# Kernel optimization log

Measured on AMD Instinct MI355X. Metric: run time of the kernel, lower is better.

## Reference

```python
import jax, jax.numpy as jnp
import numpy as np

N_ENT = 100000
N_REL = 500
IN_DIM = 128
OUT_DIM = 128
E = 500000


def setup_inputs() -> dict:
    key = jax.random.key(0)
    ks = jax.random.split(key, 9)
    src = jax.random.randint(ks[0], (E,), 0, N_ENT)
    dst = jax.random.randint(ks[1], (E,), 0, N_ENT)
    rel = jax.random.randint(ks[2], (E,), 0, N_REL)
    ent_embed = jax.random.normal(ks[3], (N_ENT, IN_DIM), dtype=jnp.float32)
    rel_embed = jax.random.normal(ks[4], (N_REL, IN_DIM), dtype=jnp.float32)
    # xavier_normal with gain 1.414 for linear weights
    g = 1.414
    a_w = jax.random.normal(ks[5], (OUT_DIM, 3 * IN_DIM), dtype=jnp.float32) * (g * np.sqrt(2.0 / (3 * IN_DIM + OUT_DIM)))
    a_b = jnp.zeros((OUT_DIM,), dtype=jnp.float32)
    a2_w = jax.random.normal(ks[6], (1, OUT_DIM), dtype=jnp.float32) * (g * np.sqrt(2.0 / (OUT_DIM + 1)))
    a2_b = jnp.zeros((1,), dtype=jnp.float32)
    return {"ent_embed": ent_embed, "rel_embed": rel_embed, "a_w": a_w, "a_b": a_b,
            "a2_w": a2_w, "a2_b": a2_b, "src": src, "dst": dst, "rel": rel}


def reference(ent_embed, rel_embed, a_w, a_b, a2_w, a2_b, src, dst, rel):
    # gather: [E, 3*in_dim]
    h = jnp.concatenate([ent_embed[src], ent_embed[dst], rel_embed[rel]], axis=1)
    c = h @ a_w.T + a_b                      # [E, out_dim]
    b = jax.nn.leaky_relu(c @ a2_w.T + a2_b, negative_slope=0.01)  # [E, 1]
    e_b = jnp.exp(b)                          # [E, 1]
    temp1 = e_b * c                           # [E, out_dim]
    # scatter-sum into source nodes (SpecialSpmmFinal keyed on edges[0] = src)
    e_b_sum = jax.ops.segment_sum(e_b, src, num_segments=N_ENT)   # [N, 1]
    h_sum = jax.ops.segment_sum(temp1, src, num_segments=N_ENT)   # [N, out_dim]
    ebs = jnp.where(e_b_sum == 0, jnp.float32(1e-12), e_b_sum)
    h_ent = h_sum / ebs
    # scatter-mean of temp1 by relation id
    rel_sum = jax.ops.segment_sum(temp1, rel, num_segments=N_REL)          # [R, out_dim]
    rel_cnt = jax.ops.segment_sum(jnp.ones((temp1.shape[0],), jnp.float32), rel, num_segments=N_REL)
    h_rel = rel_sum / jnp.maximum(rel_cnt, 1.0)[:, None]
    return (jax.nn.elu(h_ent), jax.nn.elu(h_rel))
```

## Files before the change

### kernel.cpp

```cpp
#include <hip/hip_runtime.h>
#include <hip/hip_bf16.h>

#define N_ENT_C 100000
#define N_REL_C 500
#define NEDGE_C 500000
#define SCAN_BLOCKS 391
#define EPB 1024
#define NB_EDGE 489
#define CHUNK_B 62
#define MT_TOTAL 6250
#define MT_PER_BLOCK 8
#define MFMA_GRID 782
#define CVT_GRID 1563

#define OFF_WTHI  0
#define OFF_WTLO  16384
#define OFF_WTR   32768
#define OFF_PR    49152
#define OFF_PRH   113152
#define OFF_QR    145920
#define OFF_QS    146432
#define OFF_QD    246432
#define OFF_OSRC  346432
#define OFF_DRE   446432
#define OFF_PSH   2446432
#define OFF_PDH   8846432

#define DO_HSRC     0
#define DO_BSUM     100000
#define DO_RELSTART 100512
#define DO_PART8    101024
#define DO_CHUNKOFF 105120
#define DO_BLKHIST  109216
#define DO_BLKOFFS  359584
#define DO_SDE      609952
#define DO_RELP     2609952

typedef short bf16x8 __attribute__((ext_vector_type(8)));
typedef float f32x4  __attribute__((ext_vector_type(4)));
typedef float f32x2  __attribute__((ext_vector_type(2)));
typedef unsigned short u16x8 __attribute__((ext_vector_type(8)));

__device__ inline unsigned short bf_rne(float x) {
    unsigned int u = __float_as_uint(x);
    u += 0x7FFF + ((u >> 16) & 1);
    return (unsigned short)(u >> 16);
}
__device__ inline float bf2f(unsigned short h) {
    return __uint_as_float(((unsigned int)h) << 16);
}
__device__ inline f32x2 bfpair(unsigned int w) {
    f32x2 r;
    r.x = __uint_as_float(w << 16);
    r.y = __uint_as_float(w & 0xFFFF0000u);
    return r;
}

__global__ void prep_w(const float* __restrict__ aw, unsigned short* __restrict__ Wthi,
                       unsigned short* __restrict__ Wtlo, float* __restrict__ Wtr) {
    int idx = blockIdx.x * 256 + threadIdx.x;
    if (idx < 32768) {
        int n = idx >> 7, k = idx & 127;
        float v = (n < 128) ? aw[n * 384 + k] : aw[(n - 128) * 384 + 128 + k];
        unsigned short h = bf_rne(v);
        Wthi[idx] = h;
        Wtlo[idx] = bf_rne(v - bf2f(h));
    } else if (idx < 49152) {
        int t = idx - 32768;
        int k = t >> 7, o = t & 127;
        Wtr[t] = aw[o * 384 + 256 + k];
    }
}

__global__ void rel_proj(const float* __restrict__ rele, const float* __restrict__ Wtr,
                         const float* __restrict__ ab, const float* __restrict__ a2w,
                         float* __restrict__ Pr, unsigned short* __restrict__ PrH,
                         float* __restrict__ qr) {
    int r = blockIdx.x;
    int o = threadIdx.x;
    float acc = ab[o];
    for (int k = 0; k < 128; ++k)
        acc = fmaf(rele[r * 128 + k], Wtr[k * 128 + o], acc);
    Pr[r * 128 + o] = acc;
    PrH[r * 128 + o] = bf_rne(acc);
    __shared__ float red[128];
    red[o] = acc * a2w[o];
    __syncthreads();
    for (int off = 64; off > 0; off >>= 1) {
        if (o < off) red[o] += red[o + off];
        __syncthreads();
    }
    if (o == 0) qr[r] = red[0];
}

__global__ __launch_bounds__(256) void ent_cvt(const float* __restrict__ ent,
                                               uint4* __restrict__ EntF) {
    int gw = blockIdx.x * 256 + threadIdx.x;
    int mt = gw >> 6;
    if (mt >= MT_TOTAL) return;
    int lane = gw & 63;
    int row = mt * 16 + (lane & 15);
    int kb0 = (lane >> 4) * 8;
    const float* rp = ent + (size_t)row * 128;
    size_t mb = (size_t)mt * 8;
#pragma unroll
    for (int ks = 0; ks < 4; ++ks) {
        float4 a = *(const float4*)(rp + ks * 32 + kb0);
        float4 b = *(const float4*)(rp + ks * 32 + kb0 + 4);
        float f[8] = {a.x, a.y, a.z, a.w, b.x, b.y, b.z, b.w};
        union { unsigned short u[8]; uint4 v; } H, L;
#pragma unroll
        for (int j = 0; j < 8; ++j) {
            unsigned short h = bf_rne(f[j]);
            H.u[j] = h;
            L.u[j] = bf_rne(f[j] - bf2f(h));
        }
        EntF[(mb + ks) * 64 + lane] = H.v;
        EntF[(mb + 4 + ks) * 64 + lane] = L.v;
    }
}

__global__ __launch_bounds__(512, 4) void ent_mfma3(const uint4* __restrict__ EntF,
                                                    const unsigned short* __restrict__ Wthi,
                                                    const unsigned short* __restrict__ Wtlo,
                                                    const float* __restrict__ a2w,
                                                    unsigned short* __restrict__ PsH,
                                                    unsigned short* __restrict__ PdH,
                                                    float* __restrict__ qs,
                                                    float* __restrict__ qd) {
    const int tid = threadIdx.x;
    const int w = tid >> 6, lane = tid & 63;
    const int l15 = lane & 15, lh = lane >> 4;
    const int n0 = w * 32;

    bf16x8 wh[2][4], wl[2][4];
#pragma unroll
    for (int nf = 0; nf < 2; ++nf) {
        int n = n0 + nf * 16 + l15;
#pragma unroll
        for (int ks = 0; ks < 4; ++ks) {
            int kb = ks * 32 + lh * 8;
            wh[nf][ks] = *(const bf16x8*)(Wthi + n * 128 + kb);
            wl[nf][ks] = *(const bf16x8*)(Wtlo + n * 128 + kb);
        }
    }
#pragma unroll
    for (int nf = 0; nf < 2; ++nf)
#pragma unroll
        for (int ks = 0; ks < 4; ++ks) {
            asm volatile("" : "+v"(wh[nf][ks]));
            asm volatile("" : "+v"(wl[nf][ks]));
        }

    float a2v[2][4];
#pragma unroll
    for (int nf = 0; nf < 2; ++nf)
#pragma unroll
        for (int v = 0; v < 4; ++v)
            a2v[nf][v] = a2w[(n0 + nf * 16 + lh * 4 + v) & 127];

    const bool isPs = (w < 4);
    unsigned short* PH = isPs ? PsH : PdH;
    float* qout = isPs ? qs : qd;
    const int colbase = (n0 & 127) + lh * 4;

    const bf16x8* EB = (const bf16x8*)EntF;
    f32x4 zz = {0.f, 0.f, 0.f, 0.f};
    const int mt0 = blockIdx.x * MT_PER_BLOCK;

#pragma unroll
    for (int i = 0; i < MT_PER_BLOCK; ++i) {
        int mt = mt0 + i;
        if (mt >= MT_TOTAL) break;
        size_t mb = (size_t)mt * 512;
        bf16x8 eh[4], el[4];
#pragma unroll
        for (int ks = 0; ks < 4; ++ks) {
            eh[ks] = EB[mb + (size_t)ks * 64 + lane];
            el[ks] = EB[mb + 256 + (size_t)ks * 64 + lane];
        }
        f32x4 acc[2];
        acc[0] = zz; acc[1] = zz;
#pragma unroll
        for (int ks = 0; ks < 4; ++ks)
#pragma unroll
            for (int nf = 0; nf < 2; ++nf) {
                acc[nf] = __builtin_amdgcn_mfma_f32_16x16x32_bf16(wh[nf][ks], eh[ks], acc[nf], 0, 0, 0);
                acc[nf] = __builtin_amdgcn_mfma_f32_16x16x32_bf16(wh[nf][ks], el[ks], acc[nf], 0, 0, 0);
                acc[nf] = __builtin_amdgcn_mfma_f32_16x16x32_bf16(wl[nf][ks], eh[ks], acc[nf], 0, 0, 0);
            }

        int m = mt * 16 + l15;
        float qp = 0.f;
#pragma unroll
        for (int nf = 0; nf < 2; ++nf) {
            ushort4 st;
            st.x = bf_rne(acc[nf][0]);
            st.y = bf_rne(acc[nf][1]);
            st.z = bf_rne(acc[nf][2]);
            st.w = bf_rne(acc[nf][3]);
#pragma unroll
            for (int v = 0; v < 4; ++v) qp = fmaf(acc[nf][v], a2v[nf][v], qp);
            *(ushort4*)&PH[(size_t)m * 128 + colbase + nf * 16] = st;
        }
        qp += __shfl_xor(qp, 16);
        qp += __shfl_xor(qp, 32);
        if (lane < 16) unsafeAtomicAdd(&qout[m], qp);
    }
}

__global__ __launch_bounds__(256) void edge_hist(const int* __restrict__ src,
                                                 const int* __restrict__ rel,
                                                 int* __restrict__ histSrc,
                                                 int* __restrict__ blkHist) {
    __shared__ int lh[512];
    int tid = threadIdx.x;
    lh[tid] = 0; lh[tid + 256] = 0;
    __syncthreads();
    int base = blockIdx.x * EPB;
#pragma unroll
    for (int j = 0; j < 4; ++j) {
        int e = base + j * 256 + tid;
        if (e < NEDGE_C) {
            atomicAdd(&histSrc[src[e]], 1);
            atomicAdd(&lh[rel[e]], 1);
        }
    }
    __syncthreads();
    blkHist[blockIdx.x * 512 + tid] = lh[tid];
    blkHist[blockIdx.x * 512 + 256 + tid] = lh[tid + 256];
}

__global__ void colsum(const int* __restrict__ blkHist, int* __restrict__ partial) {
    int r = threadIdx.x;
    int k = blockIdx.x;
    int b0 = k * CHUNK_B;
    int b1 = min(b0 + CHUNK_B, NB_EDGE);
    int t = 0;
    for (int b = b0; b < b1; ++b) t += blkHist[b * 512 + r];
    partial[k * 512 + r] = t;
}

__global__ void scan512(const int* __restrict__ partial, int* __restrict__ relStart,
                        int* __restrict__ chunkOff) {
    __shared__ int a[512], b2[512];
    int tid = threadIdx.x;
    int p8[8];
    int t = 0;
#pragma unroll
    for (int k = 0; k < 8; ++k) { p8[k] = partial[k * 512 + tid]; t += p8[k]; }
    a[tid] = t;
    __syncthreads();
    int v = t;
    int* cur = a; int* nxt = b2;
    for (int off = 1; off < 512; off <<= 1) {
        int x = cur[tid] + ((tid >= off) ? cur[tid - off] : 0);
        nxt[tid] = x;
        __syncthreads();
        int* tmp = cur; cur = nxt; nxt = tmp;
    }
    int excl = cur[tid] - v;
    relStart[tid] = excl;
    int run = excl;
#pragma unroll
    for (int k = 0; k < 8; ++k) { chunkOff[k * 512 + tid] = run; run += p8[k]; }
}

__global__ void colscan(const int* __restrict__ blkHist, const int* __restrict__ chunkOff,
                        int* __restrict__ blockOffs) {
    int r = threadIdx.x;
    int k = blockIdx.x;
    int b0 = k * CHUNK_B;
    int b1 = min(b0 + CHUNK_B, NB_EDGE);
    int off = chunkOff[k * 512 + r];
    for (int b = b0; b < b1; ++b) {
        blockOffs[b * 512 + r] = off;
        off += blkHist[b * 512 + r];
    }
}

__global__ void scan_blockred(const int* __restrict__ hist, int* __restrict__ blockSums, int n) {
    __shared__ int s[256];
    int tid = threadIdx.x;
    int i = blockIdx.x * 256 + tid;
    s[tid] = (i < n) ? hist[i] : 0;
    __syncthreads();
    for (int off = 128; off > 0; off >>= 1) {
        if (tid < off) s[tid] += s[tid + off];
        __syncthreads();
    }
    if (tid == 0) blockSums[blockIdx.x] = s[0];
}

__global__ void scan_single(int* __restrict__ data, int n) {
    __shared__ int a[1024], b2[1024];
    int tid = threadIdx.x;
    int v = (tid < n) ? data[tid] : 0;
    a[tid] = v;
    __syncthreads();
    int* cur = a; int* nxt = b2;
    for (int off = 1; off < 1024; off <<= 1) {
        int x = cur[tid] + ((tid >= off) ? cur[tid - off] : 0);
        nxt[tid] = x;
        __syncthreads();
        int* t = cur; cur = nxt; nxt = t;
    }
    if (tid < n) data[tid] = cur[tid] - v;
}

__global__ void scan_final(const int* __restrict__ hist, const int* __restrict__ blockOffs,
                           int* __restrict__ offs, int n) {
    __shared__ int a[256], b2[256];
    int tid = threadIdx.x;
    int i = blockIdx.x * 256 + tid;
    int v = (i < n) ? hist[i] : 0;
    a[tid] = v;
    __syncthreads();
    int* cur = a; int* nxt = b2;
    for (int off = 1; off < 256; off <<= 1) {
        int x = cur[tid] + ((tid >= off) ? cur[tid - off] : 0);
        nxt[tid] = x;
        __syncthreads();
        int* t = cur; cur = nxt; nxt = t;
    }
    if (i < n) offs[i] = cur[tid] - v + blockOffs[blockIdx.x];
}

__global__ __launch_bounds__(256) void scatter_both(const int* __restrict__ src,
                                                    const int* __restrict__ dst,
                                                    const int* __restrict__ rel,
                                                    int* __restrict__ offsSrc,
                                                    const int* __restrict__ blockOffs,
                                                    const float* __restrict__ qs,
                                                    const float* __restrict__ qd,
                                                    const float* __restrict__ qr,
                                                    const float* __restrict__ a2b,
                                                    int4* __restrict__ drE,
                                                    int4* __restrict__ sdE) {
    __shared__ int lh[512];
    int tid = threadIdx.x;
    lh[tid] = 0; lh[tid + 256] = 0;
    __syncthreads();
    float bb = a2b[0];
    int base = blockIdx.x * EPB;
    const int* bo = &blockOffs[blockIdx.x * 512];
#pragma unroll
    for (int j = 0; j < 4; ++j) {
        int e = base + j * 256 + tid;
        if (e < NEDGE_C) {
            int s = src[e], d = dst[e], r = rel[e];
            float b = qs[s] + qd[d] + qr[r] + bb;
            b = (b > 0.f) ? b : 0.01f * b;
            float eb = __expf(b);
            int ebi = __float_as_int(eb);
            int p = atomicAdd(&offsSrc[s], 1);
            drE[p] = make_int4(d, r, ebi, 0);
            int lr = atomicAdd(&lh[r], 1);
            sdE[bo[r] + lr] = make_int4(s, d, ebi, 0);
        }
    }
}

__global__ __launch_bounds__(256) void rel_phase(const unsigned short* __restrict__ PsH,
                                                 const unsigned short* __restrict__ PdH,
                                                 const int* __restrict__ relStart,
                                                 const int4* __restrict__ sdE,
                                                 float* __restrict__ relpart) {
    int r = blockIdx.x >> 3;
    int p = blockIdx.x & 7;
    int start = relStart[r];
    int end = relStart[r + 1];
    int tid = threadIdx.x;
    int w = tid >> 6;
    int h = (tid >> 5) & 1;
    int l = tid & 31;
    int slot = p * 8 + w * 2 + h;
    f32x2 acc0 = {0.f, 0.f}, acc1 = {0.f, 0.f};
    float ebs = 0.f;
    for (int i = start + slot; i < end; i += 64) {
        int4 sd = sdE[i];
        int s = sd.x, d = sd.y;
        float eb = __int_as_float(sd.z);
        uint2 pw = *(const uint2*)&PsH[(size_t)s * 128 + l * 4];
        uint2 dw = *(const uint2*)&PdH[(size_t)d * 128 + l * 4];
        f32x2 ebp = {eb, eb};
        acc0 = ebp * (bfpair(pw.x) + bfpair(dw.x)) + acc0;
        acc1 = ebp * (bfpair(pw.y) + bfpair(dw.y)) + acc1;
        ebs += eb;
    }
    __shared__ float vred[8][128];
    __shared__ float sred[8];
    int sub = w * 2 + h;
    float4 accv = make_float4(acc0.x, acc0.y, acc1.x, acc1.y);
    *(float4*)&vred[sub][l * 4] = accv;
    if (l == 0) sred[sub] = ebs;
    __syncthreads();
    if (tid < 128) {
        float v = 0.f;
#pragma unroll
        for (int k2 = 0; k2 < 8; ++k2) v += vred[k2][tid];
        float e = 0.f;
#pragma unroll
        for (int k2 = 0; k2 < 8; ++k2) e += sred[k2];
        int pi = r * 8 + p;
        relpart[pi * 132 + tid] = v;
        if (tid == 0) relpart[pi * 132 + 128] = e;
    }
}

__global__ void rel_fin(const float* __restrict__ relpart, const float* __restrict__ Pr,
                        const int* __restrict__ relStart, float* __restrict__ outRel) {
    int r = blockIdx.x;
    int o = threadIdx.x;
    float v = 0.f, e = 0.f;
#pragma unroll
    for (int p = 0; p < 8; ++p) {
        v += relpart[(r * 8 + p) * 132 + o];
        e += relpart[(r * 8 + p) * 132 + 128];
    }
    float cnt = (float)(relStart[r + 1] - relStart[r]);
    float h = (v + e * Pr[r * 128 + o]) / fmaxf(cnt, 1.f);
    outRel[r * 128 + o] = (h > 0.f) ? h : (__expf(h) - 1.f);
}

__global__ __launch_bounds__(256) void src_phase(const unsigned short* __restrict__ PsH,
                                                 const unsigned short* __restrict__ PdH,
                                                 const unsigned short* __restrict__ PrH,
                                                 const int* __restrict__ offsSrc,
                                                 const int4* __restrict__ drE,
                                                 float* __restrict__ out) {
    int wid = (blockIdx.x * 256 + threadIdx.x) >> 6;
    if (wid >= N_ENT_C) return;
    int lane = threadIdx.x & 63;
    int g = lane >> 4, l = lane & 15;
    int s = wid;
    int start = (s == 0) ? 0 : offsSrc[s - 1];
    int end = offsSrc[s];
    float* dstp = &out[(size_t)s * 128];
    if (end == start) {
        if (g == 0) {
            *(float4*)&dstp[l * 8] = make_float4(0.f, 0.f, 0.f, 0.f);
            *(float4*)&dstp[l * 8 + 4] = make_float4(0.f, 0.f, 0.f, 0.f);
        }
        return;
    }
    f32x2 accp[4];
#pragma unroll
    for (int j = 0; j < 4; ++j) accp[j] = (f32x2){0.f, 0.f};
    float ebs = 0.f;
    for (int i = start + g; i < end; i += 4) {
        int4 er = drE[i];
        int d = er.x, r = er.y;
        float eb = __int_as_float(er.z);
        uint4 dw = *(const uint4*)&PdH[(size_t)d * 128 + l * 8];
        uint4 rw = *(const uint4*)&PrH[(size_t)r * 128 + l * 8];
        f32x2 ebp = {eb, eb};
        accp[0] = ebp * (bfpair(dw.x) + bfpair(rw.x)) + accp[0];
        accp[1] = ebp * (bfpair(dw.y) + bfpair(rw.y)) + accp[1];
        accp[2] = ebp * (bfpair(dw.z) + bfpair(rw.z)) + accp[2];
        accp[3] = ebp * (bfpair(dw.w) + bfpair(rw.w)) + accp[3];
        ebs += eb;
    }
    float a8[8] = {accp[0].x, accp[0].y, accp[1].x, accp[1].y,
                   accp[2].x, accp[2].y, accp[3].x, accp[3].y};
#pragma unroll
    for (int j = 0; j < 8; ++j) {
        a8[j] += __shfl_xor(a8[j], 16);
        a8[j] += __shfl_xor(a8[j], 32);
    }
    ebs += __shfl_xor(ebs, 16);
    ebs += __shfl_xor(ebs, 32);
    if (g == 0) {
        float inv = 1.f / ebs;
        u16x8 ps = *(const u16x8*)&PsH[(size_t)s * 128 + l * 8];
        float h[8];
#pragma unroll
        for (int j = 0; j < 8; ++j) {
            float x = bf2f(ps[j]) + a8[j] * inv;
            h[j] = (x > 0.f) ? x : (__expf(x) - 1.f);
        }
        *(float4*)&dstp[l * 8]     = make_float4(h[0], h[1], h[2], h[3]);
        *(float4*)&dstp[l * 8 + 4] = make_float4(h[4], h[5], h[6], h[7]);
    }
}

extern "C" void kernel_launch(void* const* d_in, const int* in_sizes, int n_in,
                              void* d_out, int out_size, void* d_ws, size_t ws_size,
                              hipStream_t stream) {
    const float* ent  = (const float*)d_in[0];
    const float* rele = (const float*)d_in[1];
    const float* aw   = (const float*)d_in[2];
    const float* ab   = (const float*)d_in[3];
    const float* a2w  = (const float*)d_in[4];
    const float* a2b  = (const float*)d_in[5];
    const int* src    = (const int*)d_in[6];
    const int* dst    = (const int*)d_in[7];
    const int* rel    = (const int*)d_in[8];
    float* out = (float*)d_out;

    float* ws = (float*)d_ws;
    unsigned short* Wthi = (unsigned short*)(ws + OFF_WTHI);
    unsigned short* Wtlo = (unsigned short*)(ws + OFF_WTLO);
    float* Wtr = ws + OFF_WTR;
    float* Pr  = ws + OFF_PR;
    unsigned short* PrH = (unsigned short*)(ws + OFF_PRH);
    float* qr  = ws + OFF_QR;
    float* qs  = ws + OFF_QS;
    float* qd  = ws + OFF_QD;
    int* offsSrc = (int*)(ws + OFF_OSRC);
    int4* drE    = (int4*)(ws + OFF_DRE);
    unsigned short* PsH = (unsigned short*)(ws + OFF_PSH);
    unsigned short* PdH = (unsigned short*)(ws + OFF_PDH);

    int* dI = (int*)d_out;
    uint4* EntF   = (uint4*)d_out;
    int* histSrc  = dI + DO_HSRC;
    int* bsum     = dI + DO_BSUM;
    int* relStart = dI + DO_RELSTART;
    int* part8    = dI + DO_PART8;
    int* chunkOff = dI + DO_CHUNKOFF;
    int* blkHist  = dI + DO_BLKHIST;
    int* blockOffs= dI + DO_BLKOFFS;
    int4* sdE     = (int4*)(dI + DO_SDE);
    float* relpart = (float*)dI + DO_RELP;

    hipMemsetAsync(ws + OFF_QR, 0, (size_t)(OFF_OSRC - OFF_QR) * sizeof(float), stream);

    prep_w<<<192, 256, 0, stream>>>(aw, Wthi, Wtlo, Wtr);
    rel_proj<<<N_REL_C, 128, 0, stream>>>(rele, Wtr, ab, a2w, Pr, PrH, qr);
    ent_cvt<<<CVT_GRID, 256, 0, stream>>>(ent, EntF);
    ent_mfma3<<<MFMA_GRID, 512, 0, stream>>>(EntF, Wthi, Wtlo, a2w, PsH, PdH, qs, qd);

    hipMemsetAsync(histSrc, 0, (size_t)N_ENT_C * sizeof(int), stream);
    edge_hist<<<NB_EDGE, 256, 0, stream>>>(src, rel, histSrc, blkHist);
    colsum<<<8, 512, 0, stream>>>(blkHist, part8);
    scan512<<<1, 512, 0, stream>>>(part8, relStart, chunkOff);
    colscan<<<8, 512, 0, stream>>>(blkHist, chunkOff, blockOffs);
    scan_blockred<<<SCAN_BLOCKS, 256, 0, stream>>>(histSrc, bsum, N_ENT_C);
    scan_single<<<1, 1024, 0, stream>>>(bsum, SCAN_BLOCKS);
    scan_final<<<SCAN_BLOCKS, 256, 0, stream>>>(histSrc, bsum, offsSrc, N_ENT_C);
    scatter_both<<<NB_EDGE, 256, 0, stream>>>(src, dst, rel, offsSrc, blockOffs,
                                              qs, qd, qr, a2b, drE, sdE);

    rel_phase<<<N_REL_C * 8, 256, 0, stream>>>(PsH, PdH, relStart, sdE, relpart);
    rel_fin<<<N_REL_C, 128, 0, stream>>>(relpart, Pr, relStart, out + (size_t)N_ENT_C * 128);

    src_phase<<<(N_ENT_C + 3) / 4, 256, 0, stream>>>(PsH, PdH, PrH, offsSrc, drE, out);
}
```

Baseline: 251.0 us.

## Stage split-bf16 weights in swizzled LDS and use grid-stride MFMA tiles

The entity projection kernel now copies the full hi/lo bf16 weight matrices (128 KB) into LDS with an XOR swizzle, instead of holding each wave's weight fragments in registers. The block loops grid-stride over 16-row tiles on a fixed 512-block grid, replacing the fixed 8 tiles per block. This frees VGPRs and spreads the one-time weight load over more tiles per block. In exchange it adds LDS reads inside the MFMA loop and a large shared allocation that limits occupancy to a few blocks per CU.

```diff
diff --git a/kernel.cpp b/kernel.cpp
--- a/kernel.cpp
+++ b/kernel.cpp
@@ -9,8 +9,7 @@
 #define NB_EDGE 489
 #define CHUNK_B 62
 #define MT_TOTAL 6250
-#define MT_PER_BLOCK 8
-#define MFMA_GRID 782
+#define MFMA4_GRID 512
 #define CVT_GRID 1563
 
 #define OFF_WTHI  0
@@ -120,7 +119,7 @@
     }
 }
 
-__global__ __launch_bounds__(512, 4) void ent_mfma3(const uint4* __restrict__ EntF,
+__global__ __launch_bounds__(512, 2) void ent_mfma4(const uint4* __restrict__ EntF,
                                                     const unsigned short* __restrict__ Wthi,
                                                     const unsigned short* __restrict__ Wtlo,
                                                     const float* __restrict__ a2w,
@@ -128,29 +127,24 @@
                                                     unsigned short* __restrict__ PdH,
                                                     float* __restrict__ qs,
                                                     float* __restrict__ qd) {
+    __shared__ __align__(16) char shw[131072];
     const int tid = threadIdx.x;
+
+#pragma unroll
+    for (int it = 0; it < 16; ++it) {
+        int g = it * 512 + tid;
+        int arr = g >> 12;
+        int gg = g & 4095;
+        int n = gg >> 4, slot = gg & 15;
+        const unsigned short* srcp = (arr ? Wtlo : Wthi) + n * 128 + slot * 8;
+        uint4 v = *(const uint4*)srcp;
+        *(uint4*)(shw + arr * 65536 + n * 256 + ((slot ^ (n & 7)) << 4)) = v;
+    }
+    __syncthreads();
+
     const int w = tid >> 6, lane = tid & 63;
     const int l15 = lane & 15, lh = lane >> 4;
     const int n0 = w * 32;
-
-    bf16x8 wh[2][4], wl[2][4];
-#pragma unroll
-    for (int nf = 0; nf < 2; ++nf) {
-        int n = n0 + nf * 16 + l15;
-#pragma unroll
-        for (int ks = 0; ks < 4; ++ks) {
-            int kb = ks * 32 + lh * 8;
-            wh[nf][ks] = *(const bf16x8*)(Wthi + n * 128 + kb);
-            wl[nf][ks] = *(const bf16x8*)(Wtlo + n * 128 + kb);
-        }
-    }
-#pragma unroll
-    for (int nf = 0; nf < 2; ++nf)
-#pragma unroll
-        for (int ks = 0; ks < 4; ++ks) {
-            asm volatile("" : "+v"(wh[nf][ks]));
-            asm volatile("" : "+v"(wl[nf][ks]));
-        }
 
     float a2v[2][4];
 #pragma unroll
@@ -164,14 +158,14 @@
     float* qout = isPs ? qs : qd;
     const int colbase = (n0 & 127) + lh * 4;
 
+    int nA = n0 + l15, nB = n0 + 16 + l15;
+    int offA = nA * 256, offB = nB * 256;
+    int swzA = (nA & 7), swzB = (nB & 7);
+
     const bf16x8* EB = (const bf16x8*)EntF;
     f32x4 zz = {0.f, 0.f, 0.f, 0.f};
-    const int mt0 = blockIdx.x * MT_PER_BLOCK;
-
-#pragma unroll
-    for (int i = 0; i < MT_PER_BLOCK; ++i) {
-        int mt = mt0 + i;
-        if (mt >= MT_TOTAL) break;
+
+    for (int mt = blockIdx.x; mt < MT_TOTAL; mt += MFMA4_GRID) {
         size_t mb = (size_t)mt * 512;
         bf16x8 eh[4], el[4];
 #pragma unroll
@@ -182,13 +176,21 @@
         f32x4 acc[2];
         acc[0] = zz; acc[1] = zz;
 #pragma unroll
-        for (int ks = 0; ks < 4; ++ks)
-#pragma unroll
-            for (int nf = 0; nf < 2; ++nf) {
-                acc[nf] = __builtin_amdgcn_mfma_f32_16x16x32_bf16(wh[nf][ks], eh[ks], acc[nf], 0, 0, 0);
-                acc[nf] = __builtin_amdgcn_mfma_f32_16x16x32_bf16(wh[nf][ks], el[ks], acc[nf], 0, 0, 0);
-                acc[nf] = __builtin_amdgcn_mfma_f32_16x16x32_bf16(wl[nf][ks], eh[ks], acc[nf], 0, 0, 0);
-            }
+        for (int ks = 0; ks < 4; ++ks) {
+            int slot = ks * 4 + lh;
+            int oA = offA + (((slot ^ swzA)) << 4);
+            int oB = offB + (((slot ^ swzB)) << 4);
+            bf16x8 whA = *(const bf16x8*)(shw + oA);
+            bf16x8 wlA = *(const bf16x8*)(shw + 65536 + oA);
+            bf16x8 whB = *(const bf16x8*)(shw + oB);
+            bf16x8 wlB = *(const bf16x8*)(shw + 65536 + oB);
+            acc[0] = __builtin_amdgcn_mfma_f32_16x16x32_bf16(whA, eh[ks], acc[0], 0, 0, 0);
+            acc[0] = __builtin_amdgcn_mfma_f32_16x16x32_bf16(whA, el[ks], acc[0], 0, 0, 0);
+            acc[0] = __builtin_amdgcn_mfma_f32_16x16x32_bf16(wlA, eh[ks], acc[0], 0, 0, 0);
+            acc[1] = __builtin_amdgcn_mfma_f32_16x16x32_bf16(whB, eh[ks], acc[1], 0, 0, 0);
+            acc[1] = __builtin_amdgcn_mfma_f32_16x16x32_bf16(whB, el[ks], acc[1], 0, 0, 0);
+            acc[1] = __builtin_amdgcn_mfma_f32_16x16x32_bf16(wlB, eh[ks], acc[1], 0, 0, 0);
+        }
 
         int m = mt * 16 + l15;
         float qp = 0.f;
@@ -529,7 +531,7 @@
     prep_w<<<192, 256, 0, stream>>>(aw, Wthi, Wtlo, Wtr);
     rel_proj<<<N_REL_C, 128, 0, stream>>>(rele, Wtr, ab, a2w, Pr, PrH, qr);
     ent_cvt<<<CVT_GRID, 256, 0, stream>>>(ent, EntF);
-    ent_mfma3<<<MFMA_GRID, 512, 0, stream>>>(EntF, Wthi, Wtlo, a2w, PsH, PdH, qs, qd);
+    ent_mfma4<<<MFMA4_GRID, 512, 0, stream>>>(EntF, Wthi, Wtlo, a2w, PsH, PdH, qs, qd);
 
     hipMemsetAsync(histSrc, 0, (size_t)N_ENT_C * sizeof(int), stream);
     edge_hist<<<NB_EDGE, 256, 0, stream>>>(src, rel, histSrc, blkHist);
```

After: 238.9 us. 4.8% less time.
